# Kernel optimization log

Hardware: AMD Instinct MI355X
Metric: run time of the kernel (lower is better)

Reference implementation:

```python
import jax, jax.numpy as jnp
import numpy as np
import math

H = 1024   # num_heads (nodal_demands slice)
B0 = 64    # num_base_heads
F = 2048   # num_flows (diameter slice)
O = 2048   # num_outputs
N = 8192   # batch
NB = 6     # num_blocks


def _lin_params(key, fan_in, fan_out):
    kw, kb = jax.random.split(key)
    lim = 1.0 / math.sqrt(fan_in)
    W = jax.random.uniform(kw, (fan_out, fan_in), jnp.float32, -lim, lim)
    b = jax.random.uniform(kb, (fan_out,), jnp.float32, -lim, lim)
    return W, b


def setup_inputs() -> dict:
    key = jax.random.key(0)
    ks = jax.random.split(key, 12)
    x = jax.random.normal(ks[0], (N, H + B0 + F), jnp.float32)
    W_h0q, b_h0q = _lin_params(ks[1], B0, F)
    W_sq, b_sq = _lin_params(ks[2], H, F)
    W_h0h, b_h0h = _lin_params(ks[3], B0, H)
    W_S, b_S = _lin_params(ks[4], F, F)
    W_q0h, b_q0h = _lin_params(ks[5], F, H)
    W_out, b_out = _lin_params(ks[6], F, O)

    def stack(k, fan_in, fan_out):
        Ws, bs = zip(*[_lin_params(kk, fan_in, fan_out) for kk in jax.random.split(k, NB)])
        return jnp.stack(Ws), jnp.stack(bs)

    Wb_Aq, bb_Aq = stack(ks[7], F, F)
    Wb_Dh, bb_Dh = stack(ks[8], F, H)
    Wb_fh, bb_fh = stack(ks[9], F, H)
    Wb_hf, bb_hf = stack(ks[10], H, F)
    Wb_resq, bb_resq = stack(ks[11], F, H)
    a_hf = jnp.full((NB,), 0.25, jnp.float32)  # PReLU default init
    return {
        "x": x,
        "W_h0q": W_h0q, "b_h0q": b_h0q, "W_sq": W_sq, "b_sq": b_sq,
        "W_h0h": W_h0h, "b_h0h": b_h0h, "W_S": W_S, "b_S": b_S,
        "W_q0h": W_q0h, "b_q0h": b_q0h,
        "Wb_Aq": Wb_Aq, "bb_Aq": bb_Aq, "Wb_Dh": Wb_Dh, "bb_Dh": bb_Dh,
        "Wb_fh": Wb_fh, "bb_fh": bb_fh, "Wb_hf": Wb_hf, "bb_hf": bb_hf,
        "a_hf": a_hf, "Wb_resq": Wb_resq, "bb_resq": bb_resq,
        "W_out": W_out, "b_out": b_out,
    }


def _lin(x, W, b):
    return x @ W.T + b


def _forward(x, W_h0q, b_h0q, W_sq, b_sq, W_h0h, b_h0h, W_S, b_S,
             W_q0h, b_q0h, Wb_Aq, bb_Aq, Wb_Dh, bb_Dh, Wb_fh, bb_fh,
             Wb_hf, bb_hf, a_hf, Wb_resq, bb_resq, W_out, b_out):
    s = x[:, :H]              # nodal demands
    h0 = x[:, H:H + B0]       # base heads
    d = x[:, H + B0:]         # diameters; edge_features is the same slice
    res_h0_q = _lin(h0, W_h0q, b_h0q)                 # [N, F]
    res_s_q = _lin(s, W_sq, b_sq)                     # [N, F]
    res_h0_h = _lin(h0, W_h0h, b_h0h)                 # [N, H]
    res_S_q = jax.nn.relu(_lin(d, W_S, b_S))          # [N, F]
    q = (math.pi / 4.0) * jnp.square(d)               # [N, F]
    res_q_h = _lin(q, W_q0h, b_q0h)                   # [N, H]

    sum_q_const = res_s_q + res_h0_q                  # fused: reused every block
    sum_h_const = res_h0_h

    def block(carry, p):
        q, res_q_h = carry
        W_Aq, b_Aq, W_Dh, b_Dh, W_fh, b_fh, W_hf, b_hf, a, W_resq, b_resq = p
        A_q = _lin(q * res_S_q, W_Aq, b_Aq)                       # [N, F]
        D_h = jax.nn.relu(_lin(A_q, W_Dh, b_Dh))                  # [N, H]
        hid = A_q * (q + sum_q_const)                             # [N, F]
        h = jax.nn.relu(_lin(hid, W_fh, b_fh))                    # [N, H]
        z = _lin((h + sum_h_const + res_q_h) * D_h, W_hf, b_hf)   # [N, F]
        z = jnp.where(z >= 0, z, a * z)                           # PReLU (scalar a)
        q = q - z
        res_q_h = jax.nn.relu(_lin(q, W_resq, b_resq))
        return (q, res_q_h), None

    params = (Wb_Aq, bb_Aq, Wb_Dh, bb_Dh, Wb_fh, bb_fh, Wb_hf, bb_hf,
              a_hf, Wb_resq, bb_resq)
    (q, _), _ = jax.lax.scan(block, (q, res_q_h), params)
    return _lin(q, W_out, b_out)  # num_steps == 1 -> single prediction


def reference(x, W_h0q, b_h0q, W_sq, b_sq, W_h0h, b_h0h, W_S, b_S,
              W_q0h, b_q0h, Wb_Aq, bb_Aq, Wb_Dh, bb_Dh, Wb_fh, bb_fh,
              Wb_hf, bb_hf, a_hf, Wb_resq, bb_resq, W_out, b_out):
    return _forward(x, W_h0q, b_h0q, W_sq, b_sq, W_h0h, b_h0h, W_S, b_S,
                    W_q0h, b_q0h, Wb_Aq, bb_Aq, Wb_Dh, bb_Dh, Wb_fh, bb_fh,
                    Wb_hf, bb_hf, a_hf, Wb_resq, bb_resq, W_out, b_out)
```

## Files before the change

### kernel.cpp

```cpp
#include <hip/hip_runtime.h>
#include <cstdint>
#include <cstddef>

#define NS    8192
#define HDIM  1024
#define B0DIM 64
#define FDIM  2048
#define ODIM  2048
#define NBLK  6
#define XCOLS (HDIM + B0DIM + FDIM)

typedef __bf16 bf16_t;
typedef __bf16 bf16x8 __attribute__((ext_vector_type(8)));
typedef float  f32x4  __attribute__((ext_vector_type(4)));

__device__ inline bf16x8 cvt8(f32x4 lo, f32x4 hi) {
  bf16x8 r;
#pragma unroll
  for (int i = 0; i < 4; ++i) { r[i] = (bf16_t)lo[i]; r[i + 4] = (bf16_t)hi[i]; }
  return r;
}

__global__ __launch_bounds__(256) void ew_qinit(const float* __restrict__ x,
                                                bf16_t* __restrict__ q) {
  int t = blockIdx.x * 256 + threadIdx.x;
  int n = t >> 8;
  int j = (t & 255) << 3;
  const float* p = x + (size_t)n * XCOLS + (HDIM + B0DIM) + j;
  f32x4 lo = *(const f32x4*)p;
  f32x4 hi = *(const f32x4*)(p + 4);
  bf16x8 o;
#pragma unroll
  for (int i = 0; i < 4; ++i) {
    float a = (float)(bf16_t)lo[i];
    float b = (float)(bf16_t)hi[i];
    o[i]     = (bf16_t)(0.7853981633974483f * a * a);
    o[i + 4] = (bf16_t)(0.7853981633974483f * b * b);
  }
  *(bf16x8*)(q + (size_t)n * FDIM + j) = o;
}

__global__ __launch_bounds__(256) void ew_mul(const bf16_t* a, const bf16_t* b,
                                              bf16_t* o) {
  size_t i = (size_t)(blockIdx.x * 256 + threadIdx.x) << 3;
  bf16x8 va = *(const bf16x8*)(a + i);
  bf16x8 vb = *(const bf16x8*)(b + i);
  bf16x8 vo;
#pragma unroll
  for (int k = 0; k < 8; ++k) vo[k] = (bf16_t)((float)va[k] * (float)vb[k]);
  *(bf16x8*)(o + i) = vo;
}

__global__ __launch_bounds__(256) void ew_hid(const bf16_t* aq, const bf16_t* q,
                                              const bf16_t* sq, bf16_t* o) {
  size_t i = (size_t)(blockIdx.x * 256 + threadIdx.x) << 3;
  bf16x8 va = *(const bf16x8*)(aq + i);
  bf16x8 vq = *(const bf16x8*)(q + i);
  bf16x8 vs = *(const bf16x8*)(sq + i);
  bf16x8 vo;
#pragma unroll
  for (int k = 0; k < 8; ++k)
    vo[k] = (bf16_t)((float)va[k] * ((float)vq[k] + (float)vs[k]));
  *(bf16x8*)(o + i) = vo;
}

__global__ __launch_bounds__(256) void ew_u(const bf16_t* h, const bf16_t* sh,
                                            const bf16_t* rq, const bf16_t* dh,
                                            bf16_t* o) {
  size_t i = (size_t)(blockIdx.x * 256 + threadIdx.x) << 3;
  bf16x8 vh = *(const bf16x8*)(h + i);
  bf16x8 vs = *(const bf16x8*)(sh + i);
  bf16x8 vr = *(const bf16x8*)(rq + i);
  bf16x8 vd = *(const bf16x8*)(dh + i);
  bf16x8 vo;
#pragma unroll
  for (int k = 0; k < 8; ++k)
    vo[k] = (bf16_t)(((float)vh[k] + (float)vs[k] + (float)vr[k]) * (float)vd[k]);
  *(bf16x8*)(o + i) = vo;
}

template <int EPI, bool ABF16, bool OUTF32>
__global__ __launch_bounds__(256) void gemm_nt(
    const void* __restrict__ Av, int lda, const float* __restrict__ W, int K,
    const float* __restrict__ bias, void* __restrict__ Cv, int ldc,
    const bf16_t* __restrict__ qold, const float* __restrict__ alpha_p) {
  __shared__ __align__(16) bf16_t As[128 * 32];
  __shared__ __align__(16) bf16_t Bs[128 * 32];

  const int tid  = threadIdx.x;
  const int lane = tid & 63;
  const int wave = tid >> 6;
  const int wm   = wave & 1;
  const int wn   = wave >> 1;
  const int row0 = blockIdx.y * 128;
  const int col0 = blockIdx.x * 128;

  const int srow  = tid >> 2;
  const int spart = tid & 3;

  const size_t aoff  = (size_t)(row0 + srow) * lda + spart * 8;
  const size_t aoff2 = (size_t)(row0 + srow + 64) * lda + spart * 8;
  const float* Wg  = W + (size_t)(col0 + srow) * K + spart * 8;
  const float* Wg2 = W + (size_t)(col0 + srow + 64) * K + spart * 8;

  bf16x8* AsW0 = (bf16x8*)&As[srow * 32 + spart * 8];
  bf16x8* AsW1 = (bf16x8*)&As[(srow + 64) * 32 + spart * 8];
  bf16x8* BsW0 = (bf16x8*)&Bs[srow * 32 + spart * 8];
  bf16x8* BsW1 = (bf16x8*)&Bs[(srow + 64) * 32 + spart * 8];

  f32x4 acc[4][4];
#pragma unroll
  for (int i = 0; i < 4; ++i)
#pragma unroll
    for (int j = 0; j < 4; ++j)
#pragma unroll
      for (int r = 0; r < 4; ++r) acc[i][j][r] = 0.0f;

  const int nk = K >> 5;

  f32x4 wl0, wh0, wl1, wh1;
  f32x4 al0, ah0, al1, ah1;
  bf16x8 ba0, ba1;

  auto loadk = [&](int ko) {
    wl0 = *(const f32x4*)(Wg + ko);
    wh0 = *(const f32x4*)(Wg + ko + 4);
    wl1 = *(const f32x4*)(Wg2 + ko);
    wh1 = *(const f32x4*)(Wg2 + ko + 4);
    if (ABF16) {
      const bf16_t* Ab = (const bf16_t*)Av;
      ba0 = *(const bf16x8*)(Ab + aoff + ko);
      ba1 = *(const bf16x8*)(Ab + aoff2 + ko);
    } else {
      const float* Af = (const float*)Av;
      al0 = *(const f32x4*)(Af + aoff + ko);
      ah0 = *(const f32x4*)(Af + aoff + ko + 4);
      al1 = *(const f32x4*)(Af + aoff2 + ko);
      ah1 = *(const f32x4*)(Af + aoff2 + ko + 4);
    }
  };

  loadk(0);
  const int fr   = lane & 15;
  const int quad = lane >> 4;

  for (int kt = 0; kt < nk; ++kt) {
    __syncthreads();
    if (ABF16) { *AsW0 = ba0; *AsW1 = ba1; }
    else       { *AsW0 = cvt8(al0, ah0); *AsW1 = cvt8(al1, ah1); }
    *BsW0 = cvt8(wl0, wh0);
    *BsW1 = cvt8(wl1, wh1);
    __syncthreads();
    if (kt + 1 < nk) loadk((kt + 1) * 32);

    bf16x8 af[4], bfr[4];
#pragma unroll
    for (int mt = 0; mt < 4; ++mt)
      af[mt] = *(const bf16x8*)&As[(wm * 64 + mt * 16 + fr) * 32 + quad * 8];
#pragma unroll
    for (int nt = 0; nt < 4; ++nt)
      bfr[nt] = *(const bf16x8*)&Bs[(wn * 64 + nt * 16 + fr) * 32 + quad * 8];
#pragma unroll
    for (int mt = 0; mt < 4; ++mt)
#pragma unroll
      for (int nt = 0; nt < 4; ++nt)
        acc[mt][nt] = __builtin_amdgcn_mfma_f32_16x16x32_bf16(
            af[mt], bfr[nt], acc[mt][nt], 0, 0, 0);
  }

  float alpha = 0.0f;
  if (EPI == 3) alpha = (float)(bf16_t)alpha_p[0];
  bf16_t* Cb = (bf16_t*)Cv;
  float*  Cf = (float*)Cv;

#pragma unroll
  for (int mt = 0; mt < 4; ++mt) {
#pragma unroll
    for (int nt = 0; nt < 4; ++nt) {
      int ccol = col0 + wn * 64 + nt * 16 + fr;
      float bv = (float)(bf16_t)bias[ccol];
#pragma unroll
      for (int r = 0; r < 4; ++r) {
        int crow = row0 + wm * 64 + mt * 16 + quad * 4 + r;
        size_t idx = (size_t)crow * ldc + ccol;
        float v = acc[mt][nt][r] + bv;
        if (EPI == 1) v = v > 0.0f ? v : 0.0f;
        if (EPI == 2) v += (float)Cb[idx];
        if (EPI == 3) {
          float z = v >= 0.0f ? v : alpha * v;
          v = (float)qold[idx] - z;
        }
        if (OUTF32) Cf[idx] = v; else Cb[idx] = (bf16_t)v;
      }
    }
  }
}

static inline void gemm(int sel, const void* A, int lda, const float* W, int K,
                        const float* bias, void* C, int M, const bf16_t* qold,
                        const float* alpha, hipStream_t s) {
  dim3 grid(M / 128, NS / 128), blk(256);
  switch (sel) {
    case 0: gemm_nt<0, false, false><<<grid, blk, 0, s>>>(A, lda, W, K, bias, C, M, qold, alpha); break;
    case 1: gemm_nt<1, false, false><<<grid, blk, 0, s>>>(A, lda, W, K, bias, C, M, qold, alpha); break;
    case 2: gemm_nt<2, false, false><<<grid, blk, 0, s>>>(A, lda, W, K, bias, C, M, qold, alpha); break;
    case 3: gemm_nt<0, true,  false><<<grid, blk, 0, s>>>(A, lda, W, K, bias, C, M, qold, alpha); break;
    case 4: gemm_nt<1, true,  false><<<grid, blk, 0, s>>>(A, lda, W, K, bias, C, M, qold, alpha); break;
    case 5: gemm_nt<3, true,  false><<<grid, blk, 0, s>>>(A, lda, W, K, bias, C, M, qold, alpha); break;
    case 6: gemm_nt<0, true,  true ><<<grid, blk, 0, s>>>(A, lda, W, K, bias, C, M, qold, alpha); break;
  }
}

extern "C" void kernel_launch(void* const* d_in, const int* in_sizes, int n_in,
                              void* d_out, int out_size, void* d_ws,
                              size_t ws_size, hipStream_t stream) {
  const float* x      = (const float*)d_in[0];
  const float* W_h0q  = (const float*)d_in[1];
  const float* b_h0q  = (const float*)d_in[2];
  const float* W_sq   = (const float*)d_in[3];
  const float* b_sq   = (const float*)d_in[4];
  const float* W_h0h  = (const float*)d_in[5];
  const float* b_h0h  = (const float*)d_in[6];
  const float* W_S    = (const float*)d_in[7];
  const float* b_S    = (const float*)d_in[8];
  const float* W_q0h  = (const float*)d_in[9];
  const float* b_q0h  = (const float*)d_in[10];
  const float* Wb_Aq  = (const float*)d_in[11];
  const float* bb_Aq  = (const float*)d_in[12];
  const float* Wb_Dh  = (const float*)d_in[13];
  const float* bb_Dh  = (const float*)d_in[14];
  const float* Wb_fh  = (const float*)d_in[15];
  const float* bb_fh  = (const float*)d_in[16];
  const float* Wb_hf  = (const float*)d_in[17];
  const float* bb_hf  = (const float*)d_in[18];
  const float* a_hf   = (const float*)d_in[19];
  const float* Wb_rq  = (const float*)d_in[20];
  const float* bb_rq  = (const float*)d_in[21];
  const float* W_out  = (const float*)d_in[22];
  const float* b_out  = (const float*)d_in[23];
  float* out = (float*)d_out;

  const size_t NFb = (size_t)NS * FDIM * sizeof(bf16_t);
  const size_t NHb = (size_t)NS * HDIM * sizeof(bf16_t);
  if (ws_size < 4 * NFb + 4 * NHb) return;

  char* ws = (char*)d_ws;
  bf16_t* q     = (bf16_t*)(ws);
  bf16_t* resS  = (bf16_t*)(ws + NFb);
  bf16_t* sumq  = (bf16_t*)(ws + 2 * NFb);
  bf16_t* tF1   = (bf16_t*)(ws + 3 * NFb);
  bf16_t* resqh = (bf16_t*)(ws + 4 * NFb);
  bf16_t* sumh  = (bf16_t*)(ws + 4 * NFb + NHb);
  bf16_t* tH1   = (bf16_t*)(ws + 4 * NFb + 2 * NHb);
  bf16_t* tH2   = (bf16_t*)(ws + 4 * NFb + 3 * NHb);
  bf16_t* Aq    = (bf16_t*)d_out;

  const int NFg = NS * FDIM / 8 / 256;
  const int NHg = NS * HDIM / 8 / 256;

  ew_qinit<<<NFg, 256, 0, stream>>>(x, q);
  gemm(1, x + HDIM + B0DIM, XCOLS, W_S, FDIM, b_S, resS, FDIM, nullptr, nullptr, stream);
  gemm(0, x, XCOLS, W_sq, HDIM, b_sq, sumq, FDIM, nullptr, nullptr, stream);
  gemm(2, x + HDIM, XCOLS, W_h0q, B0DIM, b_h0q, sumq, FDIM, nullptr, nullptr, stream);
  gemm(0, x + HDIM, XCOLS, W_h0h, B0DIM, b_h0h, sumh, HDIM, nullptr, nullptr, stream);
  gemm(3, q, FDIM, W_q0h, FDIM, b_q0h, resqh, HDIM, nullptr, nullptr, stream);

  for (int b = 0; b < NBLK; ++b) {
    const float* W_Aq = Wb_Aq + (size_t)b * FDIM * FDIM;
    const float* c_Aq = bb_Aq + (size_t)b * FDIM;
    const float* W_Dh = Wb_Dh + (size_t)b * HDIM * FDIM;
    const float* c_Dh = bb_Dh + (size_t)b * HDIM;
    const float* W_fh = Wb_fh + (size_t)b * HDIM * FDIM;
    const float* c_fh = bb_fh + (size_t)b * HDIM;
    const float* W_hf = Wb_hf + (size_t)b * FDIM * HDIM;
    const float* c_hf = bb_hf + (size_t)b * FDIM;
    const float* W_r  = Wb_rq + (size_t)b * HDIM * FDIM;
    const float* c_r  = bb_rq + (size_t)b * HDIM;

    ew_mul<<<NFg, 256, 0, stream>>>(q, resS, tF1);
    gemm(3, tF1, FDIM, W_Aq, FDIM, c_Aq, Aq, FDIM, nullptr, nullptr, stream);
    gemm(4, Aq, FDIM, W_Dh, FDIM, c_Dh, tH1, HDIM, nullptr, nullptr, stream);
    ew_hid<<<NFg, 256, 0, stream>>>(Aq, q, sumq, tF1);
    gemm(4, tF1, FDIM, W_fh, FDIM, c_fh, tH2, HDIM, nullptr, nullptr, stream);
    ew_u<<<NHg, 256, 0, stream>>>(tH2, sumh, resqh, tH1, tH2);
    gemm(5, tH2, HDIM, W_hf, HDIM, c_hf, q, FDIM, q, a_hf + b, stream);
    gemm(4, q, FDIM, W_r, FDIM, c_r, resqh, HDIM, nullptr, nullptr, stream);
  }

  gemm(6, q, FDIM, W_out, FDIM, b_out, out, ODIM, nullptr, nullptr, stream);
}
```

Before: 3.286 ms.

## Pre-convert weights to bf16, fuse elementwise ops into GEMM epilogues, use LDS DMA loads

All weight matrices and the input slices are converted to bf16 once per use by separate conversion kernels, so the GEMM can read bf16 operands for both sides. The elementwise kernels (q*resS, A_q*(q+sumq), the (h+sumh+res)*D_h update) are folded into the epilogues of the producing GEMMs, which removes several full activation round trips. The GEMM main loop now uses global_load_lds direct-to-LDS loads instead of register staging, but it drops the register prefetch, so loads and MFMA work are no longer overlapped. Scratch buffers are aliased more aggressively, including parts of the output buffer.

Result: slower. 3.549 ms (+8.0%).

```diff
diff --git a/kernel.cpp b/kernel.cpp
--- a/kernel.cpp
+++ b/kernel.cpp
@@ -9,6 +9,7 @@
 #define ODIM  2048
 #define NBLK  6
 #define XCOLS (HDIM + B0DIM + FDIM)
+#define SBW   (HDIM + B0DIM)
 
 typedef __bf16 bf16_t;
 typedef __bf16 bf16x8 __attribute__((ext_vector_type(8)));
@@ -21,69 +22,72 @@
   return r;
 }
 
-__global__ __launch_bounds__(256) void ew_qinit(const float* __restrict__ x,
-                                                bf16_t* __restrict__ q) {
+__device__ __forceinline__ void gload16(bf16_t* lds, const bf16_t* g) {
+  __builtin_amdgcn_global_load_lds(
+      (const __attribute__((address_space(1))) unsigned int*)g,
+      (__attribute__((address_space(3))) unsigned int*)lds, 16, 0, 0);
+}
+
+__global__ __launch_bounds__(256) void prep(const float* __restrict__ x,
+                                            bf16_t* __restrict__ xbf,
+                                            bf16_t* __restrict__ dbf,
+                                            bf16_t* __restrict__ qo) {
   int t = blockIdx.x * 256 + threadIdx.x;
-  int n = t >> 8;
-  int j = (t & 255) << 3;
-  const float* p = x + (size_t)n * XCOLS + (HDIM + B0DIM) + j;
+  int n = t / 392;
+  int c = t - n * 392;
+  const float* p = x + (size_t)n * XCOLS + c * 8;
   f32x4 lo = *(const f32x4*)p;
   f32x4 hi = *(const f32x4*)(p + 4);
-  bf16x8 o;
-#pragma unroll
-  for (int i = 0; i < 4; ++i) {
-    float a = (float)(bf16_t)lo[i];
-    float b = (float)(bf16_t)hi[i];
-    o[i]     = (bf16_t)(0.7853981633974483f * a * a);
-    o[i + 4] = (bf16_t)(0.7853981633974483f * b * b);
-  }
-  *(bf16x8*)(q + (size_t)n * FDIM + j) = o;
-}
-
-__global__ __launch_bounds__(256) void ew_mul(const bf16_t* a, const bf16_t* b,
-                                              bf16_t* o) {
-  size_t i = (size_t)(blockIdx.x * 256 + threadIdx.x) << 3;
-  bf16x8 va = *(const bf16x8*)(a + i);
-  bf16x8 vb = *(const bf16x8*)(b + i);
-  bf16x8 vo;
-#pragma unroll
-  for (int k = 0; k < 8; ++k) vo[k] = (bf16_t)((float)va[k] * (float)vb[k]);
-  *(bf16x8*)(o + i) = vo;
-}
-
-__global__ __launch_bounds__(256) void ew_hid(const bf16_t* aq, const bf16_t* q,
-                                              const bf16_t* sq, bf16_t* o) {
-  size_t i = (size_t)(blockIdx.x * 256 + threadIdx.x) << 3;
-  bf16x8 va = *(const bf16x8*)(aq + i);
-  bf16x8 vq = *(const bf16x8*)(q + i);
-  bf16x8 vs = *(const bf16x8*)(sq + i);
-  bf16x8 vo;
-#pragma unroll
-  for (int k = 0; k < 8; ++k)
-    vo[k] = (bf16_t)((float)va[k] * ((float)vq[k] + (float)vs[k]));
-  *(bf16x8*)(o + i) = vo;
-}
-
-__global__ __launch_bounds__(256) void ew_u(const bf16_t* h, const bf16_t* sh,
-                                            const bf16_t* rq, const bf16_t* dh,
-                                            bf16_t* o) {
-  size_t i = (size_t)(blockIdx.x * 256 + threadIdx.x) << 3;
-  bf16x8 vh = *(const bf16x8*)(h + i);
-  bf16x8 vs = *(const bf16x8*)(sh + i);
-  bf16x8 vr = *(const bf16x8*)(rq + i);
-  bf16x8 vd = *(const bf16x8*)(dh + i);
-  bf16x8 vo;
-#pragma unroll
-  for (int k = 0; k < 8; ++k)
-    vo[k] = (bf16_t)(((float)vh[k] + (float)vs[k] + (float)vr[k]) * (float)vd[k]);
-  *(bf16x8*)(o + i) = vo;
-}
-
-template <int EPI, bool ABF16, bool OUTF32>
-__global__ __launch_bounds__(256) void gemm_nt(
-    const void* __restrict__ Av, int lda, const float* __restrict__ W, int K,
-    const float* __restrict__ bias, void* __restrict__ Cv, int ldc,
-    const bf16_t* __restrict__ qold, const float* __restrict__ alpha_p) {
+  if (c < 136) {
+    *(bf16x8*)(xbf + (size_t)n * SBW + c * 8) = cvt8(lo, hi);
+  } else {
+    int j = c * 8 - SBW;
+    bf16x8 od, oq;
+#pragma unroll
+    for (int i = 0; i < 4; ++i) {
+      bf16_t b0 = (bf16_t)lo[i], b1 = (bf16_t)hi[i];
+      od[i] = b0; od[i + 4] = b1;
+      float f0 = (float)b0, f1 = (float)b1;
+      oq[i]     = (bf16_t)(0.7853981633974483f * f0 * f0);
+      oq[i + 4] = (bf16_t)(0.7853981633974483f * f1 * f1);
+    }
+    *(bf16x8*)(dbf + (size_t)n * FDIM + j) = od;
+    *(bf16x8*)(qo  + (size_t)n * FDIM + j) = oq;
+  }
+}
+
+__global__ __launch_bounds__(256) void wconv4(
+    const float* __restrict__ s0, bf16_t* __restrict__ d0, int n0,
+    const float* __restrict__ s1, bf16_t* __restrict__ d1, int n1,
+    const float* __restrict__ s2, bf16_t* __restrict__ d2, int n2,
+    const float* __restrict__ s3, bf16_t* __restrict__ d3, int n3) {
+  int t = blockIdx.x * 256 + threadIdx.x;
+  const float* s; bf16_t* d;
+  if (t < n0) { s = s0 + (size_t)t * 8; d = d0 + (size_t)t * 8; }
+  else {
+    t -= n0;
+    if (t < n1) { s = s1 + (size_t)t * 8; d = d1 + (size_t)t * 8; }
+    else {
+      t -= n1;
+      if (t < n2) { s = s2 + (size_t)t * 8; d = d2 + (size_t)t * 8; }
+      else {
+        t -= n2;
+        if (t < n3) { s = s3 + (size_t)t * 8; d = d3 + (size_t)t * 8; }
+        else return;
+      }
+    }
+  }
+  f32x4 lo = *(const f32x4*)s, hi = *(const f32x4*)(s + 4);
+  *(bf16x8*)d = cvt8(lo, hi);
+}
+
+template <int EPI>
+__global__ __launch_bounds__(256) void gemm_bt(
+    const bf16_t* __restrict__ A, int lda, const bf16_t* __restrict__ W, int K,
+    const float* __restrict__ bias, bf16_t* __restrict__ C, int ldc,
+    float* __restrict__ Cf, bf16_t* __restrict__ out2,
+    const bf16_t* __restrict__ p1, const bf16_t* __restrict__ p2,
+    const float* __restrict__ alpha_p) {
   __shared__ __align__(16) bf16_t As[128 * 32];
   __shared__ __align__(16) bf16_t Bs[128 * 32];
 
@@ -95,18 +99,16 @@
   const int row0 = blockIdx.y * 128;
   const int col0 = blockIdx.x * 128;
 
-  const int srow  = tid >> 2;
-  const int spart = tid & 3;
-
-  const size_t aoff  = (size_t)(row0 + srow) * lda + spart * 8;
-  const size_t aoff2 = (size_t)(row0 + srow + 64) * lda + spart * 8;
-  const float* Wg  = W + (size_t)(col0 + srow) * K + spart * 8;
-  const float* Wg2 = W + (size_t)(col0 + srow + 64) * K + spart * 8;
-
-  bf16x8* AsW0 = (bf16x8*)&As[srow * 32 + spart * 8];
-  bf16x8* AsW1 = (bf16x8*)&As[(srow + 64) * 32 + spart * 8];
-  bf16x8* BsW0 = (bf16x8*)&Bs[srow * 32 + spart * 8];
-  bf16x8* BsW1 = (bf16x8*)&Bs[(srow + 64) * 32 + spart * 8];
+  const int srow = wave * 32 + (lane >> 2);
+  const int scol = (lane & 3) * 8;
+  const bf16_t* ga0 = A + (size_t)(row0 + srow) * lda + scol;
+  const bf16_t* ga1 = ga0 + (size_t)16 * lda;
+  const bf16_t* gb0 = W + (size_t)(col0 + srow) * K + scol;
+  const bf16_t* gb1 = gb0 + (size_t)16 * K;
+  bf16_t* la0 = &As[(wave * 32) * 32];
+  bf16_t* la1 = &As[(wave * 32 + 16) * 32];
+  bf16_t* lb0 = &Bs[(wave * 32) * 32];
+  bf16_t* lb1 = &Bs[(wave * 32 + 16) * 32];
 
   f32x4 acc[4][4];
 #pragma unroll
@@ -116,42 +118,18 @@
 #pragma unroll
       for (int r = 0; r < 4; ++r) acc[i][j][r] = 0.0f;
 
-  const int nk = K >> 5;
-
-  f32x4 wl0, wh0, wl1, wh1;
-  f32x4 al0, ah0, al1, ah1;
-  bf16x8 ba0, ba1;
-
-  auto loadk = [&](int ko) {
-    wl0 = *(const f32x4*)(Wg + ko);
-    wh0 = *(const f32x4*)(Wg + ko + 4);
-    wl1 = *(const f32x4*)(Wg2 + ko);
-    wh1 = *(const f32x4*)(Wg2 + ko + 4);
-    if (ABF16) {
-      const bf16_t* Ab = (const bf16_t*)Av;
-      ba0 = *(const bf16x8*)(Ab + aoff + ko);
-      ba1 = *(const bf16x8*)(Ab + aoff2 + ko);
-    } else {
-      const float* Af = (const float*)Av;
-      al0 = *(const f32x4*)(Af + aoff + ko);
-      ah0 = *(const f32x4*)(Af + aoff + ko + 4);
-      al1 = *(const f32x4*)(Af + aoff2 + ko);
-      ah1 = *(const f32x4*)(Af + aoff2 + ko + 4);
-    }
-  };
-
-  loadk(0);
   const int fr   = lane & 15;
   const int quad = lane >> 4;
+  const int nk   = K >> 5;
 
   for (int kt = 0; kt < nk; ++kt) {
+    const int ko = kt * 32;
     __syncthreads();
-    if (ABF16) { *AsW0 = ba0; *AsW1 = ba1; }
-    else       { *AsW0 = cvt8(al0, ah0); *AsW1 = cvt8(al1, ah1); }
-    *BsW0 = cvt8(wl0, wh0);
-    *BsW1 = cvt8(wl1, wh1);
+    gload16(la0, ga0 + ko);
+    gload16(la1, ga1 + ko);
+    gload16(lb0, gb0 + ko);
+    gload16(lb1, gb1 + ko);
     __syncthreads();
-    if (kt + 1 < nk) loadk((kt + 1) * 32);
 
     bf16x8 af[4], bfr[4];
 #pragma unroll
@@ -169,9 +147,7 @@
   }
 
   float alpha = 0.0f;
-  if (EPI == 3) alpha = (float)(bf16_t)alpha_p[0];
-  bf16_t* Cb = (bf16_t*)Cv;
-  float*  Cf = (float*)Cv;
+  if (EPI == 5) alpha = (float)(bf16_t)alpha_p[0];
 
 #pragma unroll
   for (int mt = 0; mt < 4; ++mt) {
@@ -184,31 +160,44 @@
         int crow = row0 + wm * 64 + mt * 16 + quad * 4 + r;
         size_t idx = (size_t)crow * ldc + ccol;
         float v = acc[mt][nt][r] + bv;
-        if (EPI == 1) v = v > 0.0f ? v : 0.0f;
-        if (EPI == 2) v += (float)Cb[idx];
+        if (EPI == 0) C[idx] = (bf16_t)v;
+        if (EPI == 1) C[idx] = (bf16_t)(v > 0.0f ? v : 0.0f);
+        if (EPI == 7) { v += (float)C[idx]; C[idx] = (bf16_t)v; }
+        if (EPI == 2) {
+          bf16_t rb = (bf16_t)(v > 0.0f ? v : 0.0f);
+          C[idx] = rb;
+          out2[idx] = (bf16_t)((float)rb * (float)p1[idx]);
+        }
         if (EPI == 3) {
+          bf16_t ab = (bf16_t)v;
+          C[idx] = ab;
+          out2[idx] = (bf16_t)((float)ab * ((float)p1[idx] + (float)p2[idx]));
+        }
+        if (EPI == 4) {
+          bf16_t hb = (bf16_t)(v > 0.0f ? v : 0.0f);
+          float dh = (float)C[idx];
+          C[idx] = (bf16_t)(((float)hb + (float)p1[idx] + (float)p2[idx]) * dh);
+        }
+        if (EPI == 5) {
           float z = v >= 0.0f ? v : alpha * v;
-          v = (float)qold[idx] - z;
+          bf16_t qn = (bf16_t)((float)C[idx] - z);
+          C[idx] = qn;
+          out2[idx] = (bf16_t)((float)qn * (float)p1[idx]);
         }
-        if (OUTF32) Cf[idx] = v; else Cb[idx] = (bf16_t)v;
+        if (EPI == 6) Cf[idx] = v;
       }
     }
   }
 }
 
-static inline void gemm(int sel, const void* A, int lda, const float* W, int K,
-                        const float* bias, void* C, int M, const bf16_t* qold,
-                        const float* alpha, hipStream_t s) {
+template <int EPI>
+static inline void launch_gemm(const bf16_t* A, int lda, const bf16_t* W, int K,
+                               const float* bias, void* C, int M, bf16_t* out2,
+                               const bf16_t* p1, const bf16_t* p2,
+                               const float* alpha, hipStream_t s) {
   dim3 grid(M / 128, NS / 128), blk(256);
-  switch (sel) {
-    case 0: gemm_nt<0, false, false><<<grid, blk, 0, s>>>(A, lda, W, K, bias, C, M, qold, alpha); break;
-    case 1: gemm_nt<1, false, false><<<grid, blk, 0, s>>>(A, lda, W, K, bias, C, M, qold, alpha); break;
-    case 2: gemm_nt<2, false, false><<<grid, blk, 0, s>>>(A, lda, W, K, bias, C, M, qold, alpha); break;
-    case 3: gemm_nt<0, true,  false><<<grid, blk, 0, s>>>(A, lda, W, K, bias, C, M, qold, alpha); break;
-    case 4: gemm_nt<1, true,  false><<<grid, blk, 0, s>>>(A, lda, W, K, bias, C, M, qold, alpha); break;
-    case 5: gemm_nt<3, true,  false><<<grid, blk, 0, s>>>(A, lda, W, K, bias, C, M, qold, alpha); break;
-    case 6: gemm_nt<0, true,  true ><<<grid, blk, 0, s>>>(A, lda, W, K, bias, C, M, qold, alpha); break;
-  }
+  gemm_bt<EPI><<<grid, blk, 0, s>>>(A, lda, W, K, bias, (bf16_t*)C, M,
+                                    (float*)C, out2, p1, p2, alpha);
 }
 
 extern "C" void kernel_launch(void* const* d_in, const int* in_sizes, int n_in,
@@ -238,7 +227,6 @@
   const float* bb_rq  = (const float*)d_in[21];
   const float* W_out  = (const float*)d_in[22];
   const float* b_out  = (const float*)d_in[23];
-  float* out = (float*)d_out;
 
   const size_t NFb = (size_t)NS * FDIM * sizeof(bf16_t);
   const size_t NHb = (size_t)NS * HDIM * sizeof(bf16_t);
@@ -252,40 +240,67 @@
   bf16_t* resqh = (bf16_t*)(ws + 4 * NFb);
   bf16_t* sumh  = (bf16_t*)(ws + 4 * NFb + NHb);
   bf16_t* tH1   = (bf16_t*)(ws + 4 * NFb + 2 * NHb);
-  bf16_t* tH2   = (bf16_t*)(ws + 4 * NFb + 3 * NHb);
-  bf16_t* Aq    = (bf16_t*)d_out;
-
-  const int NFg = NS * FDIM / 8 / 256;
-  const int NHg = NS * HDIM / 8 / 256;
-
-  ew_qinit<<<NFg, 256, 0, stream>>>(x, q);
-  gemm(1, x + HDIM + B0DIM, XCOLS, W_S, FDIM, b_S, resS, FDIM, nullptr, nullptr, stream);
-  gemm(0, x, XCOLS, W_sq, HDIM, b_sq, sumq, FDIM, nullptr, nullptr, stream);
-  gemm(2, x + HDIM, XCOLS, W_h0q, B0DIM, b_h0q, sumq, FDIM, nullptr, nullptr, stream);
-  gemm(0, x + HDIM, XCOLS, W_h0h, B0DIM, b_h0h, sumh, HDIM, nullptr, nullptr, stream);
-  gemm(3, q, FDIM, W_q0h, FDIM, b_q0h, resqh, HDIM, nullptr, nullptr, stream);
+  bf16_t* WS    = (bf16_t*)(ws + 4 * NFb + 3 * NHb);
+  bf16_t* xbf   = tH1;
+  bf16_t* dbf   = sumq;
+  bf16_t* AqB   = (bf16_t*)d_out;
+  bf16_t* dW    = (bf16_t*)d_out + (size_t)NS * FDIM;
+  bf16_t* tFh   = dW;
+
+  const int uFF = FDIM * FDIM / 8;
+  const int uHF = HDIM * FDIM / 8;
+  const int uQ0 = FDIM * B0DIM / 8;
+  const int uH0 = HDIM * B0DIM / 8;
+
+  prep<<<NS * 392 / 256, 256, 0, stream>>>(x, xbf, dbf, q);
+
+  wconv4<<<(uFF + 255) / 256, 256, 0, stream>>>(
+      W_S, dW, uFF, nullptr, nullptr, 0, nullptr, nullptr, 0, nullptr, nullptr, 0);
+  launch_gemm<2>(dbf, FDIM, dW, FDIM, b_S, resS, FDIM, tF1, q, nullptr, nullptr, stream);
+
+  bf16_t* dWsq = dW;
+  bf16_t* dWhq = dW + (size_t)uFF * 0 + (size_t)FDIM * HDIM;
+  bf16_t* dWhh = dWhq + (size_t)FDIM * B0DIM;
+  bf16_t* dWqh = dWhh + (size_t)HDIM * B0DIM;
+  wconv4<<<(uHF + uQ0 + uH0 + uHF + 255) / 256, 256, 0, stream>>>(
+      W_sq, dWsq, uHF, W_h0q, dWhq, uQ0, W_h0h, dWhh, uH0, W_q0h, dWqh, uHF);
+
+  launch_gemm<0>(xbf, SBW, dWsq, HDIM, b_sq, sumq, FDIM, nullptr, nullptr, nullptr, nullptr, stream);
+  launch_gemm<7>(xbf + HDIM, SBW, dWhq, B0DIM, b_h0q, sumq, FDIM, nullptr, nullptr, nullptr, nullptr, stream);
+  launch_gemm<0>(xbf + HDIM, SBW, dWhh, B0DIM, b_h0h, sumh, HDIM, nullptr, nullptr, nullptr, nullptr, stream);
+  launch_gemm<0>(q, FDIM, dWqh, FDIM, b_q0h, resqh, HDIM, nullptr, nullptr, nullptr, nullptr, stream);
+
+  bf16_t* wA = WS;
+  bf16_t* wD = WS + (size_t)FDIM * FDIM;
+  bf16_t* wF = WS;
+  bf16_t* wH = WS + (size_t)HDIM * FDIM;
+  bf16_t* wR = WS + 2 * (size_t)HDIM * FDIM;
 
   for (int b = 0; b < NBLK; ++b) {
-    const float* W_Aq = Wb_Aq + (size_t)b * FDIM * FDIM;
     const float* c_Aq = bb_Aq + (size_t)b * FDIM;
-    const float* W_Dh = Wb_Dh + (size_t)b * HDIM * FDIM;
     const float* c_Dh = bb_Dh + (size_t)b * HDIM;
-    const float* W_fh = Wb_fh + (size_t)b * HDIM * FDIM;
     const float* c_fh = bb_fh + (size_t)b * HDIM;
-    const float* W_hf = Wb_hf + (size_t)b * FDIM * HDIM;
     const float* c_hf = bb_hf + (size_t)b * FDIM;
-    const float* W_r  = Wb_rq + (size_t)b * HDIM * FDIM;
     const float* c_r  = bb_rq + (size_t)b * HDIM;
 
-    ew_mul<<<NFg, 256, 0, stream>>>(q, resS, tF1);
-    gemm(3, tF1, FDIM, W_Aq, FDIM, c_Aq, Aq, FDIM, nullptr, nullptr, stream);
-    gemm(4, Aq, FDIM, W_Dh, FDIM, c_Dh, tH1, HDIM, nullptr, nullptr, stream);
-    ew_hid<<<NFg, 256, 0, stream>>>(Aq, q, sumq, tF1);
-    gemm(4, tF1, FDIM, W_fh, FDIM, c_fh, tH2, HDIM, nullptr, nullptr, stream);
-    ew_u<<<NHg, 256, 0, stream>>>(tH2, sumh, resqh, tH1, tH2);
-    gemm(5, tH2, HDIM, W_hf, HDIM, c_hf, q, FDIM, q, a_hf + b, stream);
-    gemm(4, q, FDIM, W_r, FDIM, c_r, resqh, HDIM, nullptr, nullptr, stream);
-  }
-
-  gemm(6, q, FDIM, W_out, FDIM, b_out, out, ODIM, nullptr, nullptr, stream);
-}
+    wconv4<<<(uFF + uHF + 255) / 256, 256, 0, stream>>>(
+        Wb_Aq + (size_t)b * FDIM * FDIM, wA, uFF,
+        Wb_Dh + (size_t)b * HDIM * FDIM, wD, uHF,
+        nullptr, nullptr, 0, nullptr, nullptr, 0);
+    launch_gemm<3>(tF1, FDIM, wA, FDIM, c_Aq, AqB, FDIM, tFh, q, sumq, nullptr, stream);
+    launch_gemm<1>(AqB, FDIM, wD, FDIM, c_Dh, tH1, HDIM, nullptr, nullptr, nullptr, nullptr, stream);
+
+    wconv4<<<(3 * uHF + 255) / 256, 256, 0, stream>>>(
+        Wb_fh + (size_t)b * HDIM * FDIM, wF, uHF,
+        Wb_hf + (size_t)b * FDIM * HDIM, wH, uHF,
+        Wb_rq + (size_t)b * HDIM * FDIM, wR, uHF,
+        nullptr, nullptr, 0);
+    launch_gemm<4>(tFh, FDIM, wF, FDIM, c_fh, tH1, HDIM, nullptr, sumh, resqh, nullptr, stream);
+    launch_gemm<5>(tH1, HDIM, wH, HDIM, c_hf, q, FDIM, tF1, resS, nullptr, a_hf + b, stream);
+    launch_gemm<1>(q, FDIM, wR, FDIM, c_r, resqh, HDIM, nullptr, nullptr, nullptr, nullptr, stream);
+  }
+
+  wconv4<<<(uFF + 255) / 256, 256, 0, stream>>>(
+      W_out, WS, uFF, nullptr, nullptr, 0, nullptr, nullptr, 0, nullptr, nullptr, 0);
+  launch_gemm<6>(q, FDIM, WS, FDIM, b_out, d_out, ODIM, nullptr, nullptr, nullptr, nullptr, stream);
+}
```
